# Performance work log

Measured on AMD Instinct MI355X. Metric: run time of the kernel, lower is better.

The kernel has to match this reference:

```python
import jax, jax.numpy as jnp
import numpy as np

N_NODES = 20000
N_EDGES = 640000
NODE_DIM = 128
HIDDEN = 128
NUM_LAYERS = 3


def setup_inputs() -> dict:
    key = jax.random.key(0)
    ks = jax.random.split(key, 6)
    x = jax.random.normal(ks[0], (N_NODES, NODE_DIM), dtype=jnp.float32)
    edge_index = jax.random.randint(ks[1], (2, N_EDGES), 0, N_NODES, dtype=jnp.int64)
    s = 1.0 / np.sqrt(NODE_DIM)
    W_in = jax.random.uniform(ks[2], (NODE_DIM, HIDDEN), jnp.float32, -s, s)
    b_in = jax.random.uniform(ks[3], (HIDDEN,), jnp.float32, -s, s)
    sh = 1.0 / np.sqrt(HIDDEN)
    Ws = jax.random.uniform(ks[4], (NUM_LAYERS, HIDDEN, HIDDEN), jnp.float32, -sh, sh)
    bs = jax.random.uniform(ks[5], (NUM_LAYERS, HIDDEN), jnp.float32, -sh, sh)
    return {"x": x, "edge_index": edge_index, "W_in": W_in, "b_in": b_in, "Ws": Ws, "bs": bs}


def reference(x, edge_index, W_in, b_in, Ws, bs):
    N = x.shape[0]
    loop = jnp.arange(N, dtype=edge_index.dtype)
    src = jnp.concatenate([edge_index[0], loop])  # self-loops added (PyG GCNConv default)
    dst = jnp.concatenate([edge_index[1], loop])
    # symmetric normalization: deg computed on destination nodes
    deg = jax.ops.segment_sum(jnp.ones_like(dst, dtype=x.dtype), dst, num_segments=N)
    dis = jax.lax.rsqrt(jnp.where(deg > 0, deg, 1.0))
    norm = dis[src] * dis[dst]  # [E+N]
    h = x @ W_in + b_in
    for i in range(Ws.shape[0]):
        xw = h @ Ws[i]                              # [N, H]
        msg = xw[src] * norm[:, None]               # gather + scale
        agg = jax.ops.segment_sum(msg, dst, num_segments=N) + bs[i]
        h = jax.nn.relu(agg)                        # dropout p=0 -> identity
    return h
```

## Files before the change

kernel.cpp:

```cpp
#include <hip/hip_runtime.h>
#include <hip/hip_bf16.h>


#define HDIM 128
#define SCAN_TILE 1024

typedef __attribute__((ext_vector_type(8))) short s8v;
typedef __attribute__((ext_vector_type(4))) float f4v;

__device__ __forceinline__ ushort f2bf(float f) {
    uint u = __float_as_uint(f);
    u += 0x7FFFu + ((u >> 16) & 1u);
    return (ushort)(u >> 16);
}
__device__ __forceinline__ float bf2f(ushort h) {
    return __uint_as_float(((uint)h) << 16);
}

__global__ __launch_bounds__(256) void k_count(const int* __restrict__ dst,
                                               int* __restrict__ off, int E) {
    int e = blockIdx.x * 256 + threadIdx.x;
    if (e < E) atomicAdd(&off[dst[e]], 1);
}

__global__ __launch_bounds__(256) void k_scan_blk(int* __restrict__ off,
                                                  float* __restrict__ dis,
                                                  int* __restrict__ bsum, int N) {
    int t = threadIdx.x;
    int base = blockIdx.x * SCAN_TILE + t * 4;
    int4 d = make_int4(0, 0, 0, 0);
    if (base + 3 < N) d = *(const int4*)(off + base);
    else {
        if (base + 0 < N) d.x = off[base + 0];
        if (base + 1 < N) d.y = off[base + 1];
        if (base + 2 < N) d.z = off[base + 2];
    }
    if (base + 0 < N) dis[base + 0] = rsqrtf((float)(d.x + 1));
    if (base + 1 < N) dis[base + 1] = rsqrtf((float)(d.y + 1));
    if (base + 2 < N) dis[base + 2] = rsqrtf((float)(d.z + 1));
    if (base + 3 < N) dis[base + 3] = rsqrtf((float)(d.w + 1));

    int tsum = d.x + d.y + d.z + d.w;
    int lane = t & 63;
    int incl = tsum;
    #pragma unroll
    for (int ofs = 1; ofs < 64; ofs <<= 1) {
        int u = __shfl_up(incl, ofs);
        if (lane >= ofs) incl += u;
    }
    __shared__ int wsum[4];
    if (lane == 63) wsum[t >> 6] = incl;
    __syncthreads();
    int w = t >> 6;
    int woff = 0;
    for (int i = 0; i < w; ++i) woff += wsum[i];

    int run = woff + incl - tsum;
    if (base + 0 < N) off[base + 0] = run; run += d.x;
    if (base + 1 < N) off[base + 1] = run; run += d.y;
    if (base + 2 < N) off[base + 2] = run; run += d.z;
    if (base + 3 < N) off[base + 3] = run;
    if (t == 255) bsum[blockIdx.x] = woff + incl;
}

__global__ __launch_bounds__(256) void k_scan_add(int* __restrict__ off,
                                                  const int* __restrict__ bsum, int N) {
    int bid = blockIdx.x;
    if (bid == 0) return;
    int p = 0;
    for (int i = 0; i < bid; ++i) p += bsum[i];
    int base = bid * SCAN_TILE + threadIdx.x * 4;
    if (base + 3 < N) {
        int4 v = *(const int4*)(off + base);
        v.x += p; v.y += p; v.z += p; v.w += p;
        *(int4*)(off + base) = v;
    } else {
        if (base + 0 < N) off[base + 0] += p;
        if (base + 1 < N) off[base + 1] += p;
        if (base + 2 < N) off[base + 2] += p;
    }
}

__global__ __launch_bounds__(256) void k_fill(const int* __restrict__ src,
                                              const int* __restrict__ dst,
                                              int* __restrict__ off,
                                              int* __restrict__ csr, int E) {
    int e = blockIdx.x * 256 + threadIdx.x;
    if (e >= E) return;
    int pos = atomicAdd(&off[dst[e]], 1);
    csr[pos] = src[e];
}

__global__ __launch_bounds__(256) void k_pre(const float* __restrict__ W_in,
                                             const float* __restrict__ Ws,
                                             ushort* __restrict__ Wf,
                                             const float* __restrict__ x,
                                             ushort* __restrict__ hh,
                                             ushort* __restrict__ hl,
                                             int* __restrict__ off,
                                             int N, int nbN, int total4) {
    int bid = blockIdx.x;
    if (bid < nbN) {
        int i = bid * 256 + threadIdx.x;
        if (i < N) off[i] = 0;
    } else if (bid < nbN + 256) {
        int idx = (bid - nbN) * 256 + threadIdx.x;
        int m = idx >> 14;
        int e = idx & 16383;
        int k = e >> 7, col = e & 127;
        const float* srcm = (m == 0) ? W_in : (Ws + (m - 1) * 16384);
        float w = srcm[k * 128 + col];
        ushort hi = f2bf(w);
        ushort lo = f2bf(w - bf2f(hi));
        int ks = k >> 5, lk = (k >> 3) & 3, j = k & 7;
        int ct = col >> 4, lane = lk * 16 + (col & 15);
        int o = m * 32768 + (ks * 8 + ct) * 512 + lane * 8 + j;
        Wf[o] = hi;
        Wf[o + 16384] = lo;
    } else {
        int i = (bid - nbN - 256) * 256 + threadIdx.x;
        if (i >= total4) return;
        float4 v = ((const float4*)x)[i];
        ushort a0 = f2bf(v.x), a1 = f2bf(v.y), a2 = f2bf(v.z), a3 = f2bf(v.w);
        uint2 ph, pl;
        ph.x = (uint)a0 | ((uint)a1 << 16);
        ph.y = (uint)a2 | ((uint)a3 << 16);
        pl.x = (uint)f2bf(v.x - bf2f(a0)) | ((uint)f2bf(v.y - bf2f(a1)) << 16);
        pl.y = (uint)f2bf(v.z - bf2f(a2)) | ((uint)f2bf(v.w - bf2f(a3)) << 16);
        ((uint2*)hh)[i] = ph;
        ((uint2*)hl)[i] = pl;
    }
}

template<int MODE>
__global__ __launch_bounds__(256) void k_mgemm(const ushort* Ahi, const ushort* Alo,
                                               const ushort* __restrict__ Wf,
                                               const float* __restrict__ bias,
                                               const float* __restrict__ scale,
                                               ushort* xwb, ushort* outhi,
                                               ushort* outlo, int M) {
    int l = threadIdx.x & 63;
    int gw = blockIdx.x * 4 + (threadIdx.x >> 6);
    int strip = gw >> 1, ch = gw & 1;
    int r0 = strip * 16;
    int lr = l & 15, lk = l >> 4;
    int ar = r0 + lr; if (ar >= M) ar = M - 1;

    s8v ah0 = *(const s8v*)(Ahi + (long long)ar * HDIM + lk * 8);
    s8v ah1 = *(const s8v*)(Ahi + (long long)ar * HDIM + lk * 8 + 32);
    s8v ah2 = *(const s8v*)(Ahi + (long long)ar * HDIM + lk * 8 + 64);
    s8v ah3 = *(const s8v*)(Ahi + (long long)ar * HDIM + lk * 8 + 96);
    s8v al0 = *(const s8v*)(Alo + (long long)ar * HDIM + lk * 8);
    s8v al1 = *(const s8v*)(Alo + (long long)ar * HDIM + lk * 8 + 32);
    s8v al2 = *(const s8v*)(Alo + (long long)ar * HDIM + lk * 8 + 64);
    s8v al3 = *(const s8v*)(Alo + (long long)ar * HDIM + lk * 8 + 96);
    __syncthreads();

    f4v acc[4];
    #pragma unroll
    for (int c = 0; c < 4; ++c) acc[c] = (f4v){0.f, 0.f, 0.f, 0.f};

#define KSTEP(AH, AL, ksi)                                                          \
    {                                                                               \
        const ushort* wb = Wf + ((ksi) * 8 + ch * 4) * 512 + l * 8;                 \
        _Pragma("unroll")                                                           \
        for (int c = 0; c < 4; ++c) {                                               \
            s8v bh = *(const s8v*)(wb + c * 512);                                   \
            s8v bl = *(const s8v*)(wb + 16384 + c * 512);                           \
            acc[c] = __builtin_amdgcn_mfma_f32_16x16x32_bf16(AH, bh, acc[c], 0,0,0);\
            acc[c] = __builtin_amdgcn_mfma_f32_16x16x32_bf16(AH, bl, acc[c], 0,0,0);\
            acc[c] = __builtin_amdgcn_mfma_f32_16x16x32_bf16(AL, bh, acc[c], 0,0,0);\
        }                                                                           \
    }
    KSTEP(ah0, al0, 0)
    KSTEP(ah1, al1, 1)
    KSTEP(ah2, al2, 2)
    KSTEP(ah3, al3, 3)
#undef KSTEP

    if (r0 >= M) return;
    float bbv[4], sc[4];
    #pragma unroll
    for (int c = 0; c < 4; ++c) bbv[c] = bias ? bias[(ch * 4 + c) * 16 + lr] : 0.f;
    #pragma unroll
    for (int j = 0; j < 4; ++j) sc[j] = scale ? scale[r0 + lk * 4 + j] : 1.f;

    #pragma unroll
    for (int c = 0; c < 4; ++c) {
        #pragma unroll
        for (int j = 0; j < 4; ++j) {
            int row = r0 + lk * 4 + j;
            if (row >= M) continue;
            float o = (acc[c][j] + bbv[c]) * sc[j];
            if (MODE) {
                int col = (ch * 4 + c) * 16 + lr;
                ushort h = f2bf(o);
                outhi[(long long)row * HDIM + col] = h;
                outlo[(long long)row * HDIM + col] = f2bf(o - bf2f(h));
            } else {
                int cc = c * 16 + lr;
                xwb[((long long)ch * M + row) * 64 + cc] = f2bf(o);
            }
        }
    }
}

template<int LAST>
__global__ __launch_bounds__(256) void k_agg(const int* __restrict__ off,
                                             const int* __restrict__ csr,
                                             const float* __restrict__ dis,
                                             const ushort* __restrict__ xwb,
                                             const float* __restrict__ b,
                                             float* __restrict__ outf,
                                             ushort* __restrict__ outhi,
                                             ushort* __restrict__ outlo, int N) {
    int lane = threadIdx.x & 63;
    int wv = threadIdx.x >> 6;
    int t = lane & 15, q = lane >> 4;
    int sl = blockIdx.x & 1;
    const ushort* xs = xwb + (long long)sl * N * 64;
    int v0 = (blockIdx.x >> 1) * 4 + wv;
    int vstride = (gridDim.x >> 1) * 4;

    float4 bb = ((const float4*)(b + sl * 64))[t];

#define GATH(sidx)                                                          \
    {                                                                       \
        uint2 u = *(const uint2*)(xs + (long long)(sidx) * 64 + (t << 2));  \
        ax += bf2f((ushort)u.x); ay += bf2f((ushort)(u.x >> 16));           \
        az += bf2f((ushort)u.y); aw += bf2f((ushort)(u.y >> 16));           \
    }
#define SEL(c) (q == 0 ? (c).x : q == 1 ? (c).y : q == 2 ? (c).z : (c).w)

    for (int v = v0; v < N; v += vstride) {
        int start, end;
        if (v > 0) { int2 se = *(const int2*)(off + v - 1); start = se.x; end = se.y; }
        else { start = 0; end = off[0]; }
        float dv = dis[v];

        float ax = 0.f, ay = 0.f, az = 0.f, aw = 0.f;
        if (q == 0) GATH(v);

        int i = start;
        for (; i + 32 <= end; i += 32) {
            int ib = __builtin_amdgcn_readfirstlane(i);
            int4 c0 = *(const int4*)(csr + ib);
            int4 c1 = *(const int4*)(csr + ib + 4);
            int4 c2 = *(const int4*)(csr + ib + 8);
            int4 c3 = *(const int4*)(csr + ib + 12);
            int4 c4 = *(const int4*)(csr + ib + 16);
            int4 c5 = *(const int4*)(csr + ib + 20);
            int4 c6 = *(const int4*)(csr + ib + 24);
            int4 c7 = *(const int4*)(csr + ib + 28);
            int s0 = SEL(c0), s1 = SEL(c1), s2 = SEL(c2), s3 = SEL(c3);
            int s4 = SEL(c4), s5 = SEL(c5), s6 = SEL(c6), s7 = SEL(c7);
            GATH(s0); GATH(s1); GATH(s2); GATH(s3);
            GATH(s4); GATH(s5); GATH(s6); GATH(s7);
        }
        if (i + 16 <= end) {
            int ib = __builtin_amdgcn_readfirstlane(i);
            int4 c0 = *(const int4*)(csr + ib);
            int4 c1 = *(const int4*)(csr + ib + 4);
            int4 c2 = *(const int4*)(csr + ib + 8);
            int4 c3 = *(const int4*)(csr + ib + 12);
            int s0 = SEL(c0), s1 = SEL(c1), s2 = SEL(c2), s3 = SEL(c3);
            GATH(s0); GATH(s1); GATH(s2); GATH(s3);
            i += 16;
        }
        if (i + 8 <= end) {
            int ib = __builtin_amdgcn_readfirstlane(i);
            int4 c0 = *(const int4*)(csr + ib);
            int4 c1 = *(const int4*)(csr + ib + 4);
            int s0 = SEL(c0), s1 = SEL(c1);
            GATH(s0); GATH(s1);
            i += 8;
        }
        if (i + 4 <= end) {
            int ib = __builtin_amdgcn_readfirstlane(i);
            int4 c0 = *(const int4*)(csr + ib);
            int s0 = SEL(c0);
            GATH(s0);
            i += 4;
        }
        {
            int r = end - i;
            if (q < r) {
                int s = csr[__builtin_amdgcn_readfirstlane(i) + q];
                GATH(s);
            }
        }

        ax += __shfl_xor(ax, 16); ax += __shfl_xor(ax, 32);
        ay += __shfl_xor(ay, 16); ay += __shfl_xor(ay, 32);
        az += __shfl_xor(az, 16); az += __shfl_xor(az, 32);
        aw += __shfl_xor(aw, 16); aw += __shfl_xor(aw, 32);

        if (q == 0) {
            float ox = fmaxf(fmaf(dv, ax, bb.x), 0.f);
            float oy = fmaxf(fmaf(dv, ay, bb.y), 0.f);
            float oz = fmaxf(fmaf(dv, az, bb.z), 0.f);
            float ow = fmaxf(fmaf(dv, aw, bb.w), 0.f);
            long long oidx = (long long)v * HDIM + sl * 64 + (t << 2);
            if (LAST) {
                *(float4*)(outf + oidx) = make_float4(ox, oy, oz, ow);
            } else {
                ushort h0 = f2bf(ox), h1 = f2bf(oy), h2 = f2bf(oz), h3 = f2bf(ow);
                uint2 ph, pl;
                ph.x = (uint)h0 | ((uint)h1 << 16);
                ph.y = (uint)h2 | ((uint)h3 << 16);
                pl.x = (uint)f2bf(ox - bf2f(h0)) | ((uint)f2bf(oy - bf2f(h1)) << 16);
                pl.y = (uint)f2bf(oz - bf2f(h2)) | ((uint)f2bf(ow - bf2f(h3)) << 16);
                *(uint2*)(outhi + oidx) = ph;
                *(uint2*)(outlo + oidx) = pl;
            }
        }
    }
#undef GATH
#undef SEL
}

extern "C" void kernel_launch(void* const* d_in, const int* in_sizes, int n_in,
                              void* d_out, int out_size, void* d_ws, size_t ws_size,
                              hipStream_t stream) {
    const float* x    = (const float*)d_in[0];
    const int*   ei   = (const int*)d_in[1];
    const float* W_in = (const float*)d_in[2];
    const float* b_in = (const float*)d_in[3];
    const float* Ws   = (const float*)d_in[4];
    const float* bs   = (const float*)d_in[5];

    const int N = in_sizes[0] / HDIM;
    const int E = in_sizes[1] / 2;
    const int* src = ei;
    const int* dst = ei + E;

    float*  dis = (float*)d_ws;
    int*    off = (int*)(dis + N);
    int*    csr = off + N;
    ushort* hh  = (ushort*)(csr + E);
    ushort* hl  = hh + (long long)N * HDIM;
    ushort* xwb = hl + (long long)N * HDIM;
    ushort* Wf  = (ushort*)d_out;

    int nb_N    = (N + 255) / 256;
    int nb_E    = (E + 255) / 256;
    int nb_scan = (N + SCAN_TILE - 1) / SCAN_TILE;
    int nwaves  = ((N + 15) / 16) * 2;
    int nb_mg   = (nwaves + 3) / 4;
    int total4  = N * (HDIM / 4);
    int nb_x4   = (total4 + 255) / 256;
    int nb_pre  = nb_N + 256 + nb_x4;
    int nb_agg  = 2048;

    k_pre<<<nb_pre, 256, 0, stream>>>(W_in, Ws, Wf, x, hh, hl, off, N, nb_N, total4);

    k_count   <<<nb_E,    256, 0, stream>>>(dst, off, E);
    k_scan_blk<<<nb_scan, 256, 0, stream>>>(off, dis, csr, N);
    k_scan_add<<<nb_scan, 256, 0, stream>>>(off, csr, N);
    k_fill    <<<nb_E,    256, 0, stream>>>(src, dst, off, csr, E);

    k_mgemm<1><<<nb_mg, 256, 0, stream>>>(hh, hl, Wf, b_in, nullptr,
                                          nullptr, hh, hl, N);

    for (int layer = 0; layer < 3; ++layer) {
        const ushort* Wfm = Wf + (long long)(layer + 1) * 32768;
        const float* b = bs + (long long)layer * HDIM;
        k_mgemm<0><<<nb_mg, 256, 0, stream>>>(hh, hl, Wfm, nullptr, dis,
                                              xwb, nullptr, nullptr, N);
        if (layer == 2)
            k_agg<1><<<nb_agg, 256, 0, stream>>>(off, csr, dis, xwb, b,
                                                 (float*)d_out, nullptr, nullptr, N);
        else
            k_agg<0><<<nb_agg, 256, 0, stream>>>(off, csr, dis, xwb, b,
                                                 nullptr, hh, hl, N);
    }
}
```

Before: 193.2 us.

## Stage column slabs of XW in LDS for aggregation and split degree counters

The aggregation kernel is restructured so each 1024-thread block copies a 4-column slab of the transformed features (160KB) into shared memory and gathers neighbours from LDS, with 32 column groups times 8 node chunks as the grid. The GEMM output layout changes to column-pair-major to match. Edge counting and CSR fill now process four edges per thread and use four interleaved counters per node to cut atomic contention, with the scan extended over them. This trades the random global gathers for repeated slab loads and low occupancy, since only one block fits per CU.

Measured after the change: 467.3 us. 2.42x slower.

```diff
diff --git a/kernel.cpp b/kernel.cpp
--- a/kernel.cpp
+++ b/kernel.cpp
@@ -3,7 +3,6 @@
 
 
 #define HDIM 128
-#define SCAN_TILE 1024
 
 typedef __attribute__((ext_vector_type(8))) short s8v;
 typedef __attribute__((ext_vector_type(4))) float f4v;
@@ -16,30 +15,36 @@
 __device__ __forceinline__ float bf2f(ushort h) {
     return __uint_as_float(((uint)h) << 16);
 }
+__device__ __forceinline__ float bflo(uint u) {
+    return __uint_as_float(u << 16);
+}
+__device__ __forceinline__ float bfhi(uint u) {
+    return __uint_as_float(u & 0xFFFF0000u);
+}
+
 
 __global__ __launch_bounds__(256) void k_count(const int* __restrict__ dst,
-                                               int* __restrict__ off, int E) {
-    int e = blockIdx.x * 256 + threadIdx.x;
-    if (e < E) atomicAdd(&off[dst[e]], 1);
-}
-
-__global__ __launch_bounds__(256) void k_scan_blk(int* __restrict__ off,
+                                               int* __restrict__ off4, int E4) {
+    int t = blockIdx.x * 256 + threadIdx.x;
+    if (t >= E4) return;
+    int4 d = ((const int4*)dst)[t];
+    atomicAdd(&off4[d.x * 4 + 0], 1);
+    atomicAdd(&off4[d.y * 4 + 1], 1);
+    atomicAdd(&off4[d.z * 4 + 2], 1);
+    atomicAdd(&off4[d.w * 4 + 3], 1);
+}
+
+__global__ __launch_bounds__(256) void k_scan_blk(int* __restrict__ off4,
                                                   float* __restrict__ dis,
                                                   int* __restrict__ bsum, int N) {
     int t = threadIdx.x;
-    int base = blockIdx.x * SCAN_TILE + t * 4;
+    int total = N * 4;
+    int base = blockIdx.x * 1024 + t * 4;
     int4 d = make_int4(0, 0, 0, 0);
-    if (base + 3 < N) d = *(const int4*)(off + base);
-    else {
-        if (base + 0 < N) d.x = off[base + 0];
-        if (base + 1 < N) d.y = off[base + 1];
-        if (base + 2 < N) d.z = off[base + 2];
-    }
-    if (base + 0 < N) dis[base + 0] = rsqrtf((float)(d.x + 1));
-    if (base + 1 < N) dis[base + 1] = rsqrtf((float)(d.y + 1));
-    if (base + 2 < N) dis[base + 2] = rsqrtf((float)(d.z + 1));
-    if (base + 3 < N) dis[base + 3] = rsqrtf((float)(d.w + 1));
-
+    if (base < total) {
+        d = *(const int4*)(off4 + base);
+        dis[base >> 2] = rsqrtf((float)(d.x + d.y + d.z + d.w + 1));
+    }
     int tsum = d.x + d.y + d.z + d.w;
     int lane = t & 63;
     int incl = tsum;
@@ -56,39 +61,41 @@
     for (int i = 0; i < w; ++i) woff += wsum[i];
 
     int run = woff + incl - tsum;
-    if (base + 0 < N) off[base + 0] = run; run += d.x;
-    if (base + 1 < N) off[base + 1] = run; run += d.y;
-    if (base + 2 < N) off[base + 2] = run; run += d.z;
-    if (base + 3 < N) off[base + 3] = run;
+    if (base < total) {
+        off4[base + 0] = run; run += d.x;
+        off4[base + 1] = run; run += d.y;
+        off4[base + 2] = run; run += d.z;
+        off4[base + 3] = run;
+    }
     if (t == 255) bsum[blockIdx.x] = woff + incl;
 }
 
-__global__ __launch_bounds__(256) void k_scan_add(int* __restrict__ off,
+__global__ __launch_bounds__(256) void k_scan_add(int* __restrict__ off4,
                                                   const int* __restrict__ bsum, int N) {
     int bid = blockIdx.x;
     if (bid == 0) return;
     int p = 0;
     for (int i = 0; i < bid; ++i) p += bsum[i];
-    int base = bid * SCAN_TILE + threadIdx.x * 4;
-    if (base + 3 < N) {
-        int4 v = *(const int4*)(off + base);
+    int base = bid * 1024 + threadIdx.x * 4;
+    if (base < N * 4) {
+        int4 v = *(const int4*)(off4 + base);
         v.x += p; v.y += p; v.z += p; v.w += p;
-        *(int4*)(off + base) = v;
-    } else {
-        if (base + 0 < N) off[base + 0] += p;
-        if (base + 1 < N) off[base + 1] += p;
-        if (base + 2 < N) off[base + 2] += p;
+        *(int4*)(off4 + base) = v;
     }
 }
 
 __global__ __launch_bounds__(256) void k_fill(const int* __restrict__ src,
                                               const int* __restrict__ dst,
-                                              int* __restrict__ off,
-                                              int* __restrict__ csr, int E) {
-    int e = blockIdx.x * 256 + threadIdx.x;
-    if (e >= E) return;
-    int pos = atomicAdd(&off[dst[e]], 1);
-    csr[pos] = src[e];
+                                              int* __restrict__ off4,
+                                              int* __restrict__ csr, int E4) {
+    int t = blockIdx.x * 256 + threadIdx.x;
+    if (t >= E4) return;
+    int4 s = ((const int4*)src)[t];
+    int4 d = ((const int4*)dst)[t];
+    int p0 = atomicAdd(&off4[d.x * 4 + 0], 1); csr[p0] = s.x;
+    int p1 = atomicAdd(&off4[d.y * 4 + 1], 1); csr[p1] = s.y;
+    int p2 = atomicAdd(&off4[d.z * 4 + 2], 1); csr[p2] = s.z;
+    int p3 = atomicAdd(&off4[d.w * 4 + 3], 1); csr[p3] = s.w;
 }
 
 __global__ __launch_bounds__(256) void k_pre(const float* __restrict__ W_in,
@@ -97,14 +104,14 @@
                                              const float* __restrict__ x,
                                              ushort* __restrict__ hh,
                                              ushort* __restrict__ hl,
-                                             int* __restrict__ off,
-                                             int N, int nbN, int total4) {
+                                             int* __restrict__ off4,
+                                             int N, int nbZ, int total4) {
     int bid = blockIdx.x;
-    if (bid < nbN) {
+    if (bid < nbZ) {
         int i = bid * 256 + threadIdx.x;
-        if (i < N) off[i] = 0;
-    } else if (bid < nbN + 256) {
-        int idx = (bid - nbN) * 256 + threadIdx.x;
+        if (i < N * 4) off4[i] = 0;
+    } else if (bid < nbZ + 256) {
+        int idx = (bid - nbZ) * 256 + threadIdx.x;
         int m = idx >> 14;
         int e = idx & 16383;
         int k = e >> 7, col = e & 127;
@@ -118,7 +125,7 @@
         Wf[o] = hi;
         Wf[o + 16384] = lo;
     } else {
-        int i = (bid - nbN - 256) * 256 + threadIdx.x;
+        int i = (bid - nbZ - 256) * 256 + threadIdx.x;
         if (i >= total4) return;
         float4 v = ((const float4*)x)[i];
         ushort a0 = f2bf(v.x), a1 = f2bf(v.y), a2 = f2bf(v.z), a3 = f2bf(v.w);
@@ -192,131 +199,110 @@
             int row = r0 + lk * 4 + j;
             if (row >= M) continue;
             float o = (acc[c][j] + bbv[c]) * sc[j];
+            int col = (ch * 4 + c) * 16 + lr;
             if (MODE) {
-                int col = (ch * 4 + c) * 16 + lr;
                 ushort h = f2bf(o);
                 outhi[(long long)row * HDIM + col] = h;
                 outlo[(long long)row * HDIM + col] = f2bf(o - bf2f(h));
             } else {
-                int cc = c * 16 + lr;
-                xwb[((long long)ch * M + row) * 64 + cc] = f2bf(o);
+                int cp2 = col >> 1, ci = col & 1;
+                xwb[((long long)cp2 * M + row) * 2 + ci] = f2bf(o);
             }
         }
     }
 }
 
 template<int LAST>
-__global__ __launch_bounds__(256) void k_agg(const int* __restrict__ off,
-                                             const int* __restrict__ csr,
-                                             const float* __restrict__ dis,
-                                             const ushort* __restrict__ xwb,
-                                             const float* __restrict__ b,
-                                             float* __restrict__ outf,
-                                             ushort* __restrict__ outhi,
-                                             ushort* __restrict__ outlo, int N) {
+__global__ __launch_bounds__(1024) void k_agg(const int* __restrict__ off4,
+                                              const int* __restrict__ csr,
+                                              const float* __restrict__ dis,
+                                              const ushort* __restrict__ xwb,
+                                              const float* __restrict__ b,
+                                              float* __restrict__ outf,
+                                              ushort* __restrict__ outhi,
+                                              ushort* __restrict__ outlo,
+                                              int N, int chunkN) {
+    __shared__ uint xl4[40000];
+    int g = blockIdx.x & 31;
+    int chunk = blockIdx.x >> 5;
+
+    {
+        const float4* s4 = (const float4*)(xwb + (long long)g * N * 4);
+        float4* d4 = (float4*)xl4;
+        int tot = N / 2;
+        for (int i = threadIdx.x; i < tot; i += 1024) d4[i] = s4[i];
+    }
+    __syncthreads();
+
     int lane = threadIdx.x & 63;
     int wv = threadIdx.x >> 6;
-    int t = lane & 15, q = lane >> 4;
-    int sl = blockIdx.x & 1;
-    const ushort* xs = xwb + (long long)sl * N * 64;
-    int v0 = (blockIdx.x >> 1) * 4 + wv;
-    int vstride = (gridDim.x >> 1) * 4;
-
-    float4 bb = ((const float4*)(b + sl * 64))[t];
-
-#define GATH(sidx)                                                          \
-    {                                                                       \
-        uint2 u = *(const uint2*)(xs + (long long)(sidx) * 64 + (t << 2));  \
-        ax += bf2f((ushort)u.x); ay += bf2f((ushort)(u.x >> 16));           \
-        az += bf2f((ushort)u.y); aw += bf2f((ushort)(u.y >> 16));           \
-    }
-#define SEL(c) (q == 0 ? (c).x : q == 1 ? (c).y : q == 2 ? (c).z : (c).w)
-
-    for (int v = v0; v < N; v += vstride) {
-        int start, end;
-        if (v > 0) { int2 se = *(const int2*)(off + v - 1); start = se.x; end = se.y; }
-        else { start = 0; end = off[0]; }
-        float dv = dis[v];
-
-        float ax = 0.f, ay = 0.f, az = 0.f, aw = 0.f;
-        if (q == 0) GATH(v);
-
-        int i = start;
-        for (; i + 32 <= end; i += 32) {
-            int ib = __builtin_amdgcn_readfirstlane(i);
-            int4 c0 = *(const int4*)(csr + ib);
-            int4 c1 = *(const int4*)(csr + ib + 4);
-            int4 c2 = *(const int4*)(csr + ib + 8);
-            int4 c3 = *(const int4*)(csr + ib + 12);
-            int4 c4 = *(const int4*)(csr + ib + 16);
-            int4 c5 = *(const int4*)(csr + ib + 20);
-            int4 c6 = *(const int4*)(csr + ib + 24);
-            int4 c7 = *(const int4*)(csr + ib + 28);
-            int s0 = SEL(c0), s1 = SEL(c1), s2 = SEL(c2), s3 = SEL(c3);
-            int s4 = SEL(c4), s5 = SEL(c5), s6 = SEL(c6), s7 = SEL(c7);
-            GATH(s0); GATH(s1); GATH(s2); GATH(s3);
-            GATH(s4); GATH(s5); GATH(s6); GATH(s7);
+    int cpp = lane & 1;
+    int q = (lane >> 1) & 15;
+    int half = lane >> 5;
+    int half32 = half << 5;
+    int hl5 = lane & 31;
+
+    int base = chunk * chunkN;
+    int limit = min(N, base + chunkN);
+    int per = (chunkN + 15) >> 4;
+    int wlo = base + wv * per;
+    int whiW = min(wlo + per, limit);
+
+    float bbx = b[g * 4 + cpp * 2];
+    float bby = b[g * 4 + cpp * 2 + 1];
+    const uint* slab = xl4 + cpp * N;
+
+    for (int v0 = wlo; v0 < whiW; v0 += 2) {
+        int nv = v0 + half;
+        bool actn = nv < whiW;
+        int nvc = actn ? nv : (whiW - 1);
+        int nv4 = nvc * 4;
+        int stt = (nvc > 0) ? off4[nv4 - 1] : 0;
+        int edn = off4[nv4 + 3];
+
+        uint su = slab[nvc];
+        float ax = (q == 0) ? bflo(su) : 0.f;
+        float ay = (q == 0) ? bfhi(su) : 0.f;
+
+        int pos = stt;
+        while (__any(pos < edn)) {
+            int c = csr[pos + hl5];
+            bool a0 = (pos + q) < edn;
+            bool a1 = (pos + 16 + q) < edn;
+            int s0 = __shfl(c, half32 + q);
+            int s1 = __shfl(c, half32 + 16 + q);
+            s0 = a0 ? s0 : 0;
+            s1 = a1 ? s1 : 0;
+            uint u0 = slab[s0];
+            uint u1 = slab[s1];
+            ax += a0 ? bflo(u0) : 0.f;
+            ay += a0 ? bfhi(u0) : 0.f;
+            ax += a1 ? bflo(u1) : 0.f;
+            ay += a1 ? bfhi(u1) : 0.f;
+            pos += 32;
         }
-        if (i + 16 <= end) {
-            int ib = __builtin_amdgcn_readfirstlane(i);
-            int4 c0 = *(const int4*)(csr + ib);
-            int4 c1 = *(const int4*)(csr + ib + 4);
-            int4 c2 = *(const int4*)(csr + ib + 8);
-            int4 c3 = *(const int4*)(csr + ib + 12);
-            int s0 = SEL(c0), s1 = SEL(c1), s2 = SEL(c2), s3 = SEL(c3);
-            GATH(s0); GATH(s1); GATH(s2); GATH(s3);
-            i += 16;
-        }
-        if (i + 8 <= end) {
-            int ib = __builtin_amdgcn_readfirstlane(i);
-            int4 c0 = *(const int4*)(csr + ib);
-            int4 c1 = *(const int4*)(csr + ib + 4);
-            int s0 = SEL(c0), s1 = SEL(c1);
-            GATH(s0); GATH(s1);
-            i += 8;
-        }
-        if (i + 4 <= end) {
-            int ib = __builtin_amdgcn_readfirstlane(i);
-            int4 c0 = *(const int4*)(csr + ib);
-            int s0 = SEL(c0);
-            GATH(s0);
-            i += 4;
-        }
-        {
-            int r = end - i;
-            if (q < r) {
-                int s = csr[__builtin_amdgcn_readfirstlane(i) + q];
-                GATH(s);
+
+        ax += __shfl_xor(ax, 2);  ay += __shfl_xor(ay, 2);
+        ax += __shfl_xor(ax, 4);  ay += __shfl_xor(ay, 4);
+        ax += __shfl_xor(ax, 8);  ay += __shfl_xor(ay, 8);
+        ax += __shfl_xor(ax, 16); ay += __shfl_xor(ay, 16);
+
+        if (q == 0 && actn) {
+            float dv = dis[nvc];
+            float ox = fmaxf(fmaf(dv, ax, bbx), 0.f);
+            float oy = fmaxf(fmaf(dv, ay, bby), 0.f);
+            long long col0 = g * 4 + cpp * 2;
+            if (LAST) {
+                *(float2*)(outf + (long long)nv * HDIM + col0) = make_float2(ox, oy);
+            } else {
+                ushort h0 = f2bf(ox), h1 = f2bf(oy);
+                *(uint*)(outhi + (long long)nv * HDIM + col0) =
+                    (uint)h0 | ((uint)h1 << 16);
+                *(uint*)(outlo + (long long)nv * HDIM + col0) =
+                    (uint)f2bf(ox - bf2f(h0)) | ((uint)f2bf(oy - bf2f(h1)) << 16);
             }
         }
-
-        ax += __shfl_xor(ax, 16); ax += __shfl_xor(ax, 32);
-        ay += __shfl_xor(ay, 16); ay += __shfl_xor(ay, 32);
-        az += __shfl_xor(az, 16); az += __shfl_xor(az, 32);
-        aw += __shfl_xor(aw, 16); aw += __shfl_xor(aw, 32);
-
-        if (q == 0) {
-            float ox = fmaxf(fmaf(dv, ax, bb.x), 0.f);
-            float oy = fmaxf(fmaf(dv, ay, bb.y), 0.f);
-            float oz = fmaxf(fmaf(dv, az, bb.z), 0.f);
-            float ow = fmaxf(fmaf(dv, aw, bb.w), 0.f);
-            long long oidx = (long long)v * HDIM + sl * 64 + (t << 2);
-            if (LAST) {
-                *(float4*)(outf + oidx) = make_float4(ox, oy, oz, ow);
-            } else {
-                ushort h0 = f2bf(ox), h1 = f2bf(oy), h2 = f2bf(oz), h3 = f2bf(ow);
-                uint2 ph, pl;
-                ph.x = (uint)h0 | ((uint)h1 << 16);
-                ph.y = (uint)h2 | ((uint)h3 << 16);
-                pl.x = (uint)f2bf(ox - bf2f(h0)) | ((uint)f2bf(oy - bf2f(h1)) << 16);
-                pl.y = (uint)f2bf(oz - bf2f(h2)) | ((uint)f2bf(ow - bf2f(h3)) << 16);
-                *(uint2*)(outhi + oidx) = ph;
-                *(uint2*)(outlo + oidx) = pl;
-            }
-        }
-    }
-#undef GATH
-#undef SEL
+    }
 }
 
 extern "C" void kernel_launch(void* const* d_in, const int* in_sizes, int n_in,
@@ -335,29 +321,30 @@
     const int* dst = ei + E;
 
     float*  dis = (float*)d_ws;
-    int*    off = (int*)(dis + N);
-    int*    csr = off + N;
+    int*    off4 = (int*)(dis + N);
+    int*    csr = off4 + 4 * N;
     ushort* hh  = (ushort*)(csr + E);
     ushort* hl  = hh + (long long)N * HDIM;
     ushort* xwb = hl + (long long)N * HDIM;
     ushort* Wf  = (ushort*)d_out;
 
-    int nb_N    = (N + 255) / 256;
-    int nb_E    = (E + 255) / 256;
-    int nb_scan = (N + SCAN_TILE - 1) / SCAN_TILE;
+    int nbZ     = (4 * N + 255) / 256;
+    int nb_E4   = (E / 4 + 255) / 256;
+    int nb_scan = (4 * N + 1023) / 1024;
     int nwaves  = ((N + 15) / 16) * 2;
     int nb_mg   = (nwaves + 3) / 4;
     int total4  = N * (HDIM / 4);
     int nb_x4   = (total4 + 255) / 256;
-    int nb_pre  = nb_N + 256 + nb_x4;
-    int nb_agg  = 2048;
-
-    k_pre<<<nb_pre, 256, 0, stream>>>(W_in, Ws, Wf, x, hh, hl, off, N, nb_N, total4);
-
-    k_count   <<<nb_E,    256, 0, stream>>>(dst, off, E);
-    k_scan_blk<<<nb_scan, 256, 0, stream>>>(off, dis, csr, N);
-    k_scan_add<<<nb_scan, 256, 0, stream>>>(off, csr, N);
-    k_fill    <<<nb_E,    256, 0, stream>>>(src, dst, off, csr, E);
+    int nb_pre  = nbZ + 256 + nb_x4;
+    int chunkN  = (N + 7) / 8;
+    int nb_agg  = 32 * 8;
+
+    k_pre<<<nb_pre, 256, 0, stream>>>(W_in, Ws, Wf, x, hh, hl, off4, N, nbZ, total4);
+
+    k_count   <<<nb_E4,   256, 0, stream>>>(dst, off4, E / 4);
+    k_scan_blk<<<nb_scan, 256, 0, stream>>>(off4, dis, csr, N);
+    k_scan_add<<<nb_scan, 256, 0, stream>>>(off4, csr, N);
+    k_fill    <<<nb_E4,   256, 0, stream>>>(src, dst, off4, csr, E / 4);
 
     k_mgemm<1><<<nb_mg, 256, 0, stream>>>(hh, hl, Wf, b_in, nullptr,
                                           nullptr, hh, hl, N);
@@ -368,10 +355,11 @@
         k_mgemm<0><<<nb_mg, 256, 0, stream>>>(hh, hl, Wfm, nullptr, dis,
                                               xwb, nullptr, nullptr, N);
         if (layer == 2)
-            k_agg<1><<<nb_agg, 256, 0, stream>>>(off, csr, dis, xwb, b,
-                                                 (float*)d_out, nullptr, nullptr, N);
+            k_agg<1><<<nb_agg, 1024, 0, stream>>>(off4, csr, dis, xwb, b,
+                                                  (float*)d_out, nullptr, nullptr,
+                                                  N, chunkN);
         else
-            k_agg<0><<<nb_agg, 256, 0, stream>>>(off, csr, dis, xwb, b,
-                                                 nullptr, hh, hl, N);
-    }
-}
+            k_agg<0><<<nb_agg, 1024, 0, stream>>>(off4, csr, dis, xwb, b,
+                                                  nullptr, hh, hl, N, chunkN);
+    }
+}
```

## Split degree counters into four sub-bins and record per-edge ranks for CSR fill

Applied to the files above, without the earlier changes.

Degree counting now spreads atomics across four sub-counters per node (one per int4 lane), which cuts same-address atomic contention, and it records each edge's returned rank. The fill pass then places edges with plain stores at scanned offset plus rank instead of a second round of atomics. The scan runs over the 4N sub-counters, and a sentinel entry lets aggregation read start and end directly. This adds a rank buffer and a larger offset array, and it assumes E is divisible by 4 with 16-byte aligned edge arrays.

New measurement: 169.3 us. 1.14x faster.

```diff
diff --git a/kernel.cpp b/kernel.cpp
--- a/kernel.cpp
+++ b/kernel.cpp
@@ -3,7 +3,6 @@
 
 
 #define HDIM 128
-#define SCAN_TILE 1024
 
 typedef __attribute__((ext_vector_type(8))) short s8v;
 typedef __attribute__((ext_vector_type(4))) float f4v;
@@ -17,29 +16,32 @@
     return __uint_as_float(((uint)h) << 16);
 }
 
+
 __global__ __launch_bounds__(256) void k_count(const int* __restrict__ dst,
-                                               int* __restrict__ off, int E) {
-    int e = blockIdx.x * 256 + threadIdx.x;
-    if (e < E) atomicAdd(&off[dst[e]], 1);
-}
-
-__global__ __launch_bounds__(256) void k_scan_blk(int* __restrict__ off,
+                                               int* __restrict__ off4,
+                                               int* __restrict__ rank, int E4) {
+    int t = blockIdx.x * 256 + threadIdx.x;
+    if (t >= E4) return;
+    int4 d = ((const int4*)dst)[t];
+    int4 r;
+    r.x = atomicAdd(&off4[d.x * 4 + 0], 1);
+    r.y = atomicAdd(&off4[d.y * 4 + 1], 1);
+    r.z = atomicAdd(&off4[d.z * 4 + 2], 1);
+    r.w = atomicAdd(&off4[d.w * 4 + 3], 1);
+    ((int4*)rank)[t] = r;
+}
+
+__global__ __launch_bounds__(256) void k_scan_blk(int* __restrict__ off4,
                                                   float* __restrict__ dis,
                                                   int* __restrict__ bsum, int N) {
     int t = threadIdx.x;
-    int base = blockIdx.x * SCAN_TILE + t * 4;
+    int total = N * 4;
+    int base = blockIdx.x * 1024 + t * 4;
     int4 d = make_int4(0, 0, 0, 0);
-    if (base + 3 < N) d = *(const int4*)(off + base);
-    else {
-        if (base + 0 < N) d.x = off[base + 0];
-        if (base + 1 < N) d.y = off[base + 1];
-        if (base + 2 < N) d.z = off[base + 2];
-    }
-    if (base + 0 < N) dis[base + 0] = rsqrtf((float)(d.x + 1));
-    if (base + 1 < N) dis[base + 1] = rsqrtf((float)(d.y + 1));
-    if (base + 2 < N) dis[base + 2] = rsqrtf((float)(d.z + 1));
-    if (base + 3 < N) dis[base + 3] = rsqrtf((float)(d.w + 1));
-
+    if (base < total) {
+        d = *(const int4*)(off4 + base);
+        dis[base >> 2] = rsqrtf((float)(d.x + d.y + d.z + d.w + 1));
+    }
     int tsum = d.x + d.y + d.z + d.w;
     int lane = t & 63;
     int incl = tsum;
@@ -56,39 +58,47 @@
     for (int i = 0; i < w; ++i) woff += wsum[i];
 
     int run = woff + incl - tsum;
-    if (base + 0 < N) off[base + 0] = run; run += d.x;
-    if (base + 1 < N) off[base + 1] = run; run += d.y;
-    if (base + 2 < N) off[base + 2] = run; run += d.z;
-    if (base + 3 < N) off[base + 3] = run;
+    if (base < total) {
+        off4[base + 0] = run; run += d.x;
+        off4[base + 1] = run; run += d.y;
+        off4[base + 2] = run; run += d.z;
+        off4[base + 3] = run;
+    }
     if (t == 255) bsum[blockIdx.x] = woff + incl;
 }
 
-__global__ __launch_bounds__(256) void k_scan_add(int* __restrict__ off,
-                                                  const int* __restrict__ bsum, int N) {
+__global__ __launch_bounds__(256) void k_scan_add(int* __restrict__ off4,
+                                                  const int* __restrict__ bsum,
+                                                  int N, int E) {
     int bid = blockIdx.x;
-    if (bid == 0) return;
+    if (bid == 0) {
+        if (threadIdx.x == 0) off4[N * 4] = E;
+        return;
+    }
     int p = 0;
     for (int i = 0; i < bid; ++i) p += bsum[i];
-    int base = bid * SCAN_TILE + threadIdx.x * 4;
-    if (base + 3 < N) {
-        int4 v = *(const int4*)(off + base);
+    int base = bid * 1024 + threadIdx.x * 4;
+    if (base < N * 4) {
+        int4 v = *(const int4*)(off4 + base);
         v.x += p; v.y += p; v.z += p; v.w += p;
-        *(int4*)(off + base) = v;
-    } else {
-        if (base + 0 < N) off[base + 0] += p;
-        if (base + 1 < N) off[base + 1] += p;
-        if (base + 2 < N) off[base + 2] += p;
+        *(int4*)(off4 + base) = v;
     }
 }
 
 __global__ __launch_bounds__(256) void k_fill(const int* __restrict__ src,
                                               const int* __restrict__ dst,
-                                              int* __restrict__ off,
-                                              int* __restrict__ csr, int E) {
-    int e = blockIdx.x * 256 + threadIdx.x;
-    if (e >= E) return;
-    int pos = atomicAdd(&off[dst[e]], 1);
-    csr[pos] = src[e];
+                                              const int* __restrict__ off4,
+                                              const int* __restrict__ rank,
+                                              int* __restrict__ csr, int E4) {
+    int t = blockIdx.x * 256 + threadIdx.x;
+    if (t >= E4) return;
+    int4 s = ((const int4*)src)[t];
+    int4 d = ((const int4*)dst)[t];
+    int4 r = ((const int4*)rank)[t];
+    csr[off4[d.x * 4 + 0] + r.x] = s.x;
+    csr[off4[d.y * 4 + 1] + r.y] = s.y;
+    csr[off4[d.z * 4 + 2] + r.z] = s.z;
+    csr[off4[d.w * 4 + 3] + r.w] = s.w;
 }
 
 __global__ __launch_bounds__(256) void k_pre(const float* __restrict__ W_in,
@@ -97,14 +107,14 @@
                                              const float* __restrict__ x,
                                              ushort* __restrict__ hh,
                                              ushort* __restrict__ hl,
-                                             int* __restrict__ off,
-                                             int N, int nbN, int total4) {
+                                             int* __restrict__ off4,
+                                             int N, int nbZ, int total4) {
     int bid = blockIdx.x;
-    if (bid < nbN) {
+    if (bid < nbZ) {
         int i = bid * 256 + threadIdx.x;
-        if (i < N) off[i] = 0;
-    } else if (bid < nbN + 256) {
-        int idx = (bid - nbN) * 256 + threadIdx.x;
+        if (i < N * 4) off4[i] = 0;
+    } else if (bid < nbZ + 256) {
+        int idx = (bid - nbZ) * 256 + threadIdx.x;
         int m = idx >> 14;
         int e = idx & 16383;
         int k = e >> 7, col = e & 127;
@@ -118,7 +128,7 @@
         Wf[o] = hi;
         Wf[o + 16384] = lo;
     } else {
-        int i = (bid - nbN - 256) * 256 + threadIdx.x;
+        int i = (bid - nbZ - 256) * 256 + threadIdx.x;
         if (i >= total4) return;
         float4 v = ((const float4*)x)[i];
         ushort a0 = f2bf(v.x), a1 = f2bf(v.y), a2 = f2bf(v.z), a3 = f2bf(v.w);
@@ -206,7 +216,7 @@
 }
 
 template<int LAST>
-__global__ __launch_bounds__(256) void k_agg(const int* __restrict__ off,
+__global__ __launch_bounds__(256) void k_agg(const int* __restrict__ off4,
                                              const int* __restrict__ csr,
                                              const float* __restrict__ dis,
                                              const ushort* __restrict__ xwb,
@@ -233,9 +243,8 @@
 #define SEL(c) (q == 0 ? (c).x : q == 1 ? (c).y : q == 2 ? (c).z : (c).w)
 
     for (int v = v0; v < N; v += vstride) {
-        int start, end;
-        if (v > 0) { int2 se = *(const int2*)(off + v - 1); start = se.x; end = se.y; }
-        else { start = 0; end = off[0]; }
+        int start = off4[v << 2];
+        int end   = off4[(v << 2) + 4];
         float dv = dis[v];
 
         float ax = 0.f, ay = 0.f, az = 0.f, aw = 0.f;
@@ -334,30 +343,31 @@
     const int* src = ei;
     const int* dst = ei + E;
 
-    float*  dis = (float*)d_ws;
-    int*    off = (int*)(dis + N);
-    int*    csr = off + N;
-    ushort* hh  = (ushort*)(csr + E);
-    ushort* hl  = hh + (long long)N * HDIM;
-    ushort* xwb = hl + (long long)N * HDIM;
-    ushort* Wf  = (ushort*)d_out;
-
-    int nb_N    = (N + 255) / 256;
-    int nb_E    = (E + 255) / 256;
-    int nb_scan = (N + SCAN_TILE - 1) / SCAN_TILE;
+    float*  dis  = (float*)d_ws;
+    int*    off4 = (int*)(dis + N);
+    int*    csr  = off4 + 4 * N + 4;
+    int*    rank = csr + E;
+    ushort* hh   = (ushort*)(rank + E);
+    ushort* hl   = hh + (long long)N * HDIM;
+    ushort* xwb  = hl + (long long)N * HDIM;
+    ushort* Wf   = (ushort*)d_out;
+
+    int nbZ     = (4 * N + 255) / 256;
+    int nb_E4   = (E / 4 + 255) / 256;
+    int nb_scan = (4 * N + 1023) / 1024;
     int nwaves  = ((N + 15) / 16) * 2;
     int nb_mg   = (nwaves + 3) / 4;
     int total4  = N * (HDIM / 4);
     int nb_x4   = (total4 + 255) / 256;
-    int nb_pre  = nb_N + 256 + nb_x4;
+    int nb_pre  = nbZ + 256 + nb_x4;
     int nb_agg  = 2048;
 
-    k_pre<<<nb_pre, 256, 0, stream>>>(W_in, Ws, Wf, x, hh, hl, off, N, nb_N, total4);
-
-    k_count   <<<nb_E,    256, 0, stream>>>(dst, off, E);
-    k_scan_blk<<<nb_scan, 256, 0, stream>>>(off, dis, csr, N);
-    k_scan_add<<<nb_scan, 256, 0, stream>>>(off, csr, N);
-    k_fill    <<<nb_E,    256, 0, stream>>>(src, dst, off, csr, E);
+    k_pre<<<nb_pre, 256, 0, stream>>>(W_in, Ws, Wf, x, hh, hl, off4, N, nbZ, total4);
+
+    k_count   <<<nb_E4,   256, 0, stream>>>(dst, off4, rank, E / 4);
+    k_scan_blk<<<nb_scan, 256, 0, stream>>>(off4, dis, csr, N);
+    k_scan_add<<<nb_scan, 256, 0, stream>>>(off4, csr, N, E);
+    k_fill    <<<nb_E4,   256, 0, stream>>>(src, dst, off4, rank, csr, E / 4);
 
     k_mgemm<1><<<nb_mg, 256, 0, stream>>>(hh, hl, Wf, b_in, nullptr,
                                           nullptr, hh, hl, N);
@@ -368,10 +378,10 @@
         k_mgemm<0><<<nb_mg, 256, 0, stream>>>(hh, hl, Wfm, nullptr, dis,
                                               xwb, nullptr, nullptr, N);
         if (layer == 2)
-            k_agg<1><<<nb_agg, 256, 0, stream>>>(off, csr, dis, xwb, b,
+            k_agg<1><<<nb_agg, 256, 0, stream>>>(off4, csr, dis, xwb, b,
                                                  (float*)d_out, nullptr, nullptr, N);
         else
-            k_agg<0><<<nb_agg, 256, 0, stream>>>(off, csr, dis, xwb, b,
+            k_agg<0><<<nb_agg, 256, 0, stream>>>(off4, csr, dis, xwb, b,
                                                  nullptr, hh, hl, N);
     }
 }
```
